# Performance work log

Hardware: AMD Instinct MI355X
Metric: run time of the kernel (lower is better)

## Reference

```python
import jax, jax.numpy as jnp
import numpy as np

MRG = 0.1
ALPHA = 32.0
STAT_WEIGHT = 0.01
STAT_ADJUST_WEIGHT = 0.15
COS_EPS = 1e-8  # torch F.cosine_similarity eps


def l2_norm(x):
    # matches torch l2_norm: x / sqrt(sum(x^2, axis=1) + 1e-12)
    normp = jnp.sum(x * x, axis=1) + 1e-12
    return x / jnp.sqrt(normp)[:, None]


def setup_inputs() -> dict:
    key = jax.random.key(0)
    kx, kt, kp, kc = jax.random.split(key, 4)
    B, C, D = 512, 50000, 128
    X = jax.random.normal(kx, (B, D), dtype=jnp.float32)
    T = jax.random.randint(kt, (B,), 0, C, dtype=jnp.int32)
    proxies = jax.random.normal(kp, (C, D), dtype=jnp.float32)
    class_centers = jax.random.normal(kc, (C, D), dtype=jnp.float32)
    return {"X": X, "T": T, "proxies": proxies, "class_centers": class_centers}


def reference(X, T, proxies, class_centers):
    C = proxies.shape[0]
    Xn = l2_norm(X)                      # (B, D)
    Pn = l2_norm(proxies)                # (C, D)
    cos = Xn @ Pn.T                      # (B, C)

    # ---- vectorized per-class statistics (replaces the Python loop) ----
    counts = jax.ops.segment_sum(jnp.ones(T.shape[0], jnp.float32), T, num_segments=C)
    sums = jax.ops.segment_sum(Xn, T, num_segments=C)          # (C, D)
    sqs = jax.ops.segment_sum(Xn * Xn, T, num_segments=C)      # (C, D)
    safe = jnp.maximum(counts, 1.0)[:, None]
    mean = sums / safe
    var = jnp.clip(sqs / safe - mean * mean, 1e-6, 10.0)        # biased var, clamped
    var_weight = 1.0 / (1.0 + var.mean(axis=1))                 # (C,)

    # cosine_similarity(P_norm[i], class_centers[i]) with torch eps semantics
    pnorm = jnp.maximum(jnp.sqrt(jnp.sum(Pn * Pn, axis=1)), COS_EPS)
    cnorm = jnp.maximum(jnp.sqrt(jnp.sum(class_centers * class_centers, axis=1)), COS_EPS)
    center_sim = jnp.sum(Pn * class_centers, axis=1) / (pnorm * cnorm)  # (C,)

    has_samples = counts > 0
    adj = jnp.where(has_samples, center_sim * var_weight * STAT_ADJUST_WEIGHT, 0.0)
    combined = cos + adj[None, :]        # (B, C)

    # ---- proxy-anchor exp-sum terms ----
    onehot = (T[:, None] == jnp.arange(C, dtype=T.dtype)[None, :])  # (B, C) bool
    pos_exp = jnp.exp(-ALPHA * (combined - MRG))
    neg_exp = jnp.exp(ALPHA * (combined + MRG))
    P_sim_sum = jnp.sum(jnp.where(onehot, pos_exp, 0.0), axis=0)    # (C,)
    N_sim_sum = jnp.sum(jnp.where(onehot, 0.0, neg_exp), axis=0)    # (C,)

    num_valid = jnp.sum(has_samples).astype(jnp.float32)
    pos_term = jnp.sum(jnp.log1p(P_sim_sum)) / num_valid
    neg_term = jnp.sum(jnp.log1p(N_sim_sum)) / jnp.float32(C)

    center_reg = jnp.mean(jnp.abs(class_centers))
    return pos_term + neg_term + STAT_WEIGHT * center_reg
```

## Files before the change

### kernel.cpp

```cpp
#include <hip/hip_runtime.h>
#include <math.h>

#define ALPHA 32.0f
#define MRG 0.1f
#define STAT_WEIGHT 0.01f
#define STAT_ADJ_W 0.15f
#define COS_EPS 1e-8f

typedef __attribute__((ext_vector_type(8))) short bf16x8;
typedef __attribute__((ext_vector_type(4))) float f32x4;
typedef __attribute__((ext_vector_type(4))) unsigned int u32x4;

__device__ __forceinline__ ushort f2bf(float f) {
    unsigned u = __float_as_uint(f);
    return (ushort)((u + 0x7FFFu + ((u >> 16) & 1u)) >> 16);
}
__device__ __forceinline__ unsigned pk2(float a, float b) {
    return (unsigned)f2bf(a) | ((unsigned)f2bf(b) << 16);
}

__device__ __forceinline__ float bred128(float v, float* sm, int d) {
    #pragma unroll
    for (int off = 1; off < 64; off <<= 1) v += __shfl_xor(v, off);
    if ((d & 63) == 0) sm[d >> 6] = v;
    __syncthreads();
    float r = sm[0] + sm[1];
    __syncthreads();
    return r;
}

__global__ void k_stats(const float* __restrict__ X, const float* __restrict__ proxies,
                        const float* __restrict__ cc, const int* __restrict__ T,
                        ushort* __restrict__ Xn16, float* __restrict__ adj,
                        float* __restrict__ scal, int B) {
    const int b = blockIdx.x, d = threadIdx.x;
    __shared__ int Tl[512];
    __shared__ float sm[2];
    __shared__ int mlist[512];
    __shared__ int mcnt;
    for (int i = d; i < B; i += 128) Tl[i] = T[i];
    if (d == 0) mcnt = 0;
    __syncthreads();
    const int c = Tl[b];

    float x = X[(size_t)b * 128 + d];
    float n2 = bred128(x * x, sm, d);
    float xn = x * rsqrtf(n2 + 1e-12f);
    const int pk = ((((d >> 3) ^ (b & 15)) << 3) | (d & 7));
    Xn16[(size_t)b * 128 + pk] = f2bf(xn);

    for (int j = d; j < B; j += 128)
        if (Tl[j] == c) mlist[atomicAdd(&mcnt, 1)] = j;
    __syncthreads();
    const int cnt = mcnt;
    int minj = mlist[0];
    for (int i = 1; i < cnt; ++i) minj = min(minj, mlist[i]);
    if (minj != b) return;

    float sd = 0.f, qd = 0.f;
    int prev = -1;
    for (int rank = 0; rank < cnt; ++rank) {
        int cur = 0x7fffffff;
        for (int i = 0; i < cnt; ++i) { int v = mlist[i]; if (v > prev && v < cur) cur = v; }
        prev = cur;
        float xj = X[(size_t)cur * 128 + d];
        float nj = bred128(xj * xj, sm, d);
        float xnj = xj * rsqrtf(nj + 1e-12f);
        sd += xnj; qd += xnj * xnj;
    }
    float fc = (float)cnt;
    float m = sd / fc;
    float var = fminf(fmaxf(qd / fc - m * m, 1e-6f), 10.0f);
    float sv = bred128(var, sm, d);

    float p  = proxies[(size_t)c * 128 + d];
    float cv = cc[(size_t)c * 128 + d];
    float s2 = bred128(p * p, sm, d);
    float c2 = bred128(cv * cv, sm, d);
    float pc = bred128(p * cv, sm, d);
    if (d == 0) {
        float inv = rsqrtf(s2 + 1e-12f);
        float pn = fmaxf(sqrtf(s2) * inv, COS_EPS);
        float cn = fmaxf(sqrtf(c2), COS_EPS);
        float censim = (pc * inv) / (pn * cn);
        float vw = 1.0f / (1.0f + sv * (1.0f / 128.0f));
        adj[c] = censim * vw * STAT_ADJ_W;
        atomicAdd(&scal[3], 1.0f);
    }
}

__launch_bounds__(256, 2)
__global__ void k_main(const float* __restrict__ proxies, const float* __restrict__ cc,
                       const ushort* __restrict__ Xsw, const int* __restrict__ T,
                       const float* __restrict__ adj, float* __restrict__ scal,
                       float* __restrict__ out, int C, int nblk) {
    const int tid = threadIdx.x, lane = tid & 63, wv = tid >> 6;
    const int nlo = lane & 15, quad = lane >> 4;
    const int c0 = blockIdx.x * 128;

    __shared__ ushort Sx[16384];
    __shared__ int Tl[512];
    __shared__ float red[4][3];
    Tl[tid] = T[tid];
    Tl[tid + 256] = T[tid + 256];

    float cabs = 0.f;
    {
        const int n4 = ((c0 + 128 <= C) ? 128 : (C - c0)) * 32;
        const float4* cp = (const float4*)(cc + (size_t)c0 * 128);
        #pragma unroll 4
        for (int i = tid; i < n4; i += 256) {
            float4 v = cp[i];
            cabs += fabsf(v.x) + fabsf(v.y) + fabsf(v.z) + fabsf(v.w);
        }
    }

    const int cls0 = c0 + wv * 32 + nlo;
    const int cls1 = cls0 + 16;
    bf16x8 bfr[2][4];
    #pragma unroll
    for (int t = 0; t < 2; ++t) {
        int cls = c0 + wv * 32 + t * 16 + nlo;
        int cl = (cls < C) ? cls : C - 1;
        const float4* pr = (const float4*)(proxies + (size_t)cl * 128);
        float4 v0[4], v1[4];
        float s2 = 0.f;
        #pragma unroll
        for (int ks = 0; ks < 4; ++ks) {
            v0[ks] = pr[ks * 8 + quad * 2];
            v1[ks] = pr[ks * 8 + quad * 2 + 1];
            s2 += v0[ks].x*v0[ks].x + v0[ks].y*v0[ks].y + v0[ks].z*v0[ks].z + v0[ks].w*v0[ks].w
                + v1[ks].x*v1[ks].x + v1[ks].y*v1[ks].y + v1[ks].z*v1[ks].z + v1[ks].w*v1[ks].w;
        }
        s2 += __shfl_xor(s2, 16);
        s2 += __shfl_xor(s2, 32);
        float pin = rsqrtf(s2 + 1e-12f);
        #pragma unroll
        for (int ks = 0; ks < 4; ++ks) {
            u32x4 u;
            u.x = pk2(v0[ks].x * pin, v0[ks].y * pin);
            u.y = pk2(v0[ks].z * pin, v0[ks].w * pin);
            u.z = pk2(v1[ks].x * pin, v1[ks].y * pin);
            u.w = pk2(v1[ks].z * pin, v1[ks].w * pin);
            bfr[t][ks] = __builtin_bit_cast(bf16x8, u);
        }
    }

    int fro[4];
    #pragma unroll
    for (int ks = 0; ks < 4; ++ks)
        fro[ks] = nlo * 128 + (((ks * 4 + quad) ^ nlo) << 3);

    const uint4* gX = (const uint4*)Xsw;
    uint4 s0, s1, s2v, s3;
    #define LOADV(ch) { const uint4* p_ = gX + (ch) * 1024 + tid; \
                        s0 = p_[0]; s1 = p_[256]; s2v = p_[512]; s3 = p_[768]; }
    #define WRITEV(bi) { uint4* q_ = (uint4*)&Sx[(bi) * 8192]; \
                         q_[tid] = s0; q_[tid + 256] = s1; q_[tid + 512] = s2v; q_[tid + 768] = s3; }
    LOADV(0); WRITEV(0); LOADV(1);
    __syncthreads();

    float pp0 = 0.f, np0 = 0.f, pp1 = 0.f, np1 = 0.f;
    for (int chunk = 0; chunk < 8; ++chunk) {
        const int bo = (chunk & 1) * 8192;
        if (chunk < 7) {
            WRITEV((chunk + 1) & 1);
            if (chunk < 6) LOADV(chunk + 2);
        }
        #pragma unroll
        for (int rt = 0; rt < 4; ++rt) {
            const ushort* sb = &Sx[bo + rt * 2048];
            bf16x8 a0 = *(const bf16x8*)&sb[fro[0]];
            bf16x8 a1 = *(const bf16x8*)&sb[fro[1]];
            bf16x8 a2 = *(const bf16x8*)&sb[fro[2]];
            bf16x8 a3 = *(const bf16x8*)&sb[fro[3]];
            f32x4 acc0 = {0.f,0.f,0.f,0.f}, acc1 = {0.f,0.f,0.f,0.f};
            acc0 = __builtin_amdgcn_mfma_f32_16x16x32_bf16(a0, bfr[0][0], acc0, 0, 0, 0);
            acc1 = __builtin_amdgcn_mfma_f32_16x16x32_bf16(a0, bfr[1][0], acc1, 0, 0, 0);
            acc0 = __builtin_amdgcn_mfma_f32_16x16x32_bf16(a1, bfr[0][1], acc0, 0, 0, 0);
            acc1 = __builtin_amdgcn_mfma_f32_16x16x32_bf16(a1, bfr[1][1], acc1, 0, 0, 0);
            acc0 = __builtin_amdgcn_mfma_f32_16x16x32_bf16(a2, bfr[0][2], acc0, 0, 0, 0);
            acc1 = __builtin_amdgcn_mfma_f32_16x16x32_bf16(a2, bfr[1][2], acc1, 0, 0, 0);
            acc0 = __builtin_amdgcn_mfma_f32_16x16x32_bf16(a3, bfr[0][3], acc0, 0, 0, 0);
            acc1 = __builtin_amdgcn_mfma_f32_16x16x32_bf16(a3, bfr[1][3], acc1, 0, 0, 0);

            int4 t4 = *(const int4*)&Tl[chunk * 64 + rt * 16 + quad * 4];
            int tvs[4] = {t4.x, t4.y, t4.z, t4.w};
            #pragma unroll
            for (int r = 0; r < 4; ++r) {
                { bool po = (tvs[r] == cls0); float v = acc0[r];
                  float e = __expf(po ? -ALPHA * (v - MRG) : ALPHA * (v + MRG));
                  pp0 += po ? e : 0.f; np0 += po ? 0.f : e; }
                { bool po = (tvs[r] == cls1); float v = acc1[r];
                  float e = __expf(po ? -ALPHA * (v - MRG) : ALPHA * (v + MRG));
                  pp1 += po ? e : 0.f; np1 += po ? 0.f : e; }
            }
        }
        __syncthreads();
    }
    #undef LOADV
    #undef WRITEV

    pp0 += __shfl_xor(pp0, 16); pp0 += __shfl_xor(pp0, 32);
    np0 += __shfl_xor(np0, 16); np0 += __shfl_xor(np0, 32);
    pp1 += __shfl_xor(pp1, 16); pp1 += __shfl_xor(pp1, 32);
    np1 += __shfl_xor(np1, 16); np1 += __shfl_xor(np1, 32);

    float lp = 0.f, ln = 0.f;
    {
        float a0 = adj[(cls0 < C) ? cls0 : C - 1];
        float a1 = adj[(cls1 < C) ? cls1 : C - 1];
        float as0 = (pp0 > 0.f) ? a0 : 0.f;
        float as1 = (pp1 > 0.f) ? a1 : 0.f;
        if (cls0 < C) {
            lp += log1pf(pp0 * __expf(-ALPHA * as0));
            ln += log1pf(np0 * __expf( ALPHA * as0));
        }
        if (cls1 < C) {
            lp += log1pf(pp1 * __expf(-ALPHA * as1));
            ln += log1pf(np1 * __expf( ALPHA * as1));
        }
    }
    #pragma unroll
    for (int off = 1; off < 16; off <<= 1) {
        lp += __shfl_xor(lp, off);
        ln += __shfl_xor(ln, off);
    }
    #pragma unroll
    for (int off = 1; off < 64; off <<= 1) cabs += __shfl_xor(cabs, off);

    if (lane == 0) { red[wv][0] = lp; red[wv][1] = ln; red[wv][2] = cabs; }
    __syncthreads();
    if (tid == 0) {
        atomicAdd(&scal[0], red[0][0] + red[1][0] + red[2][0] + red[3][0]);
        atomicAdd(&scal[1], red[0][1] + red[1][1] + red[2][1] + red[3][1]);
        atomicAdd(&scal[2], red[0][2] + red[1][2] + red[2][2] + red[3][2]);
        __threadfence();
        unsigned old = atomicAdd((unsigned*)(scal + 4), 1u);
        if (old == (unsigned)(nblk - 1)) {
            float S0 = atomicAdd(&scal[0], 0.f);
            float S1 = atomicAdd(&scal[1], 0.f);
            float S2 = atomicAdd(&scal[2], 0.f);
            float S3 = atomicAdd(&scal[3], 0.f);
            out[0] = S0 / S3 + S1 / (float)C + STAT_WEIGHT * (S2 / ((float)C * 128.f));
        }
    }
}

extern "C" void kernel_launch(void* const* d_in, const int* in_sizes, int n_in,
                              void* d_out, int out_size, void* d_ws, size_t ws_size,
                              hipStream_t stream) {
    const float* X       = (const float*)d_in[0];
    const int*   T       = (const int*)d_in[1];
    const float* proxies = (const float*)d_in[2];
    const float* cc      = (const float*)d_in[3];
    float* out = (float*)d_out;

    const int B = in_sizes[1];
    const int D = in_sizes[0] / B;
    const int C = in_sizes[2] / D;

    float*  adj  = (float*)d_ws;
    float*  scal = adj + C;
    ushort* Xn16 = (ushort*)(scal + 8);

    const int nblk = (C + 127) / 128;

    (void)hipMemsetAsync(scal, 0, 8 * sizeof(float), stream);
    k_stats<<<B, 128, 0, stream>>>(X, proxies, cc, T, Xn16, adj, scal, B);
    k_main<<<nblk, 256, 0, stream>>>(proxies, cc, Xn16, T, adj, scal, out, C, nblk);
}
```

Measured before the change: 133.5 us.

## Split batch rows across two grid halves with atomic partial sums and finalize kernel

The main kernel's grid gains a second dimension that splits the 512 batch rows into two halves of 256. Each block now processes 4 chunks instead of 8 and atomically adds its per-class positive and negative exp sums into global buffers. A new finalize kernel applies the log1p and adjustment terms per class and does the last reduction. This doubles block count, which should help occupancy across the CUs with 391 blocks originally. The cost is per-class atomics, a larger memset and an extra kernel launch, and the proxy normalization is now done twice.

```diff
diff --git a/kernel.cpp b/kernel.cpp
--- a/kernel.cpp
+++ b/kernel.cpp
@@ -92,20 +92,21 @@
 __launch_bounds__(256, 2)
 __global__ void k_main(const float* __restrict__ proxies, const float* __restrict__ cc,
                        const ushort* __restrict__ Xsw, const int* __restrict__ T,
-                       const float* __restrict__ adj, float* __restrict__ scal,
-                       float* __restrict__ out, int C, int nblk) {
+                       float* __restrict__ Psum, float* __restrict__ Nsum,
+                       float* __restrict__ scal, int C) {
     const int tid = threadIdx.x, lane = tid & 63, wv = tid >> 6;
     const int nlo = lane & 15, quad = lane >> 4;
     const int c0 = blockIdx.x * 128;
+    const int half = blockIdx.y;
+    const int r0 = half * 256;
 
     __shared__ ushort Sx[16384];
-    __shared__ int Tl[512];
-    __shared__ float red[4][3];
-    Tl[tid] = T[tid];
-    Tl[tid + 256] = T[tid + 256];
+    __shared__ alignas(16) int Tl[256];
+    __shared__ float red[4];
+    Tl[tid] = T[r0 + tid];
 
     float cabs = 0.f;
-    {
+    if (half == 0) {
         const int n4 = ((c0 + 128 <= C) ? 128 : (C - c0)) * 32;
         const float4* cp = (const float4*)(cc + (size_t)c0 * 128);
         #pragma unroll 4
@@ -151,7 +152,7 @@
     for (int ks = 0; ks < 4; ++ks)
         fro[ks] = nlo * 128 + (((ks * 4 + quad) ^ nlo) << 3);
 
-    const uint4* gX = (const uint4*)Xsw;
+    const uint4* gX = (const uint4*)Xsw + half * 4096;
     uint4 s0, s1, s2v, s3;
     #define LOADV(ch) { const uint4* p_ = gX + (ch) * 1024 + tid; \
                         s0 = p_[0]; s1 = p_[256]; s2v = p_[512]; s3 = p_[768]; }
@@ -161,11 +162,11 @@
     __syncthreads();
 
     float pp0 = 0.f, np0 = 0.f, pp1 = 0.f, np1 = 0.f;
-    for (int chunk = 0; chunk < 8; ++chunk) {
+    for (int chunk = 0; chunk < 4; ++chunk) {
         const int bo = (chunk & 1) * 8192;
-        if (chunk < 7) {
+        if (chunk < 3) {
             WRITEV((chunk + 1) & 1);
-            if (chunk < 6) LOADV(chunk + 2);
+            if (chunk < 2) LOADV(chunk + 2);
         }
         #pragma unroll
         for (int rt = 0; rt < 4; ++rt) {
@@ -205,39 +206,47 @@
     np0 += __shfl_xor(np0, 16); np0 += __shfl_xor(np0, 32);
     pp1 += __shfl_xor(pp1, 16); pp1 += __shfl_xor(pp1, 32);
     np1 += __shfl_xor(np1, 16); np1 += __shfl_xor(np1, 32);
-
+    if (quad == 0) {
+        if (cls0 < C) { atomicAdd(&Psum[cls0], pp0); atomicAdd(&Nsum[cls0], np0); }
+        if (cls1 < C) { atomicAdd(&Psum[cls1], pp1); atomicAdd(&Nsum[cls1], np1); }
+    }
+
+    if (half == 0) {
+        #pragma unroll
+        for (int off = 1; off < 64; off <<= 1) cabs += __shfl_xor(cabs, off);
+        if (lane == 0) red[wv] = cabs;
+        __syncthreads();
+        if (tid == 0) atomicAdd(&scal[2], red[0] + red[1] + red[2] + red[3]);
+    }
+}
+
+__launch_bounds__(256)
+__global__ void k_fin(const float* __restrict__ Psum, const float* __restrict__ Nsum,
+                      const float* __restrict__ adj, float* __restrict__ scal,
+                      float* __restrict__ out, int C, int nfin) {
+    const int tid = threadIdx.x, lane = tid & 63, wv = tid >> 6;
+    const int c = blockIdx.x * 256 + tid;
+    __shared__ float red[4][2];
     float lp = 0.f, ln = 0.f;
-    {
-        float a0 = adj[(cls0 < C) ? cls0 : C - 1];
-        float a1 = adj[(cls1 < C) ? cls1 : C - 1];
-        float as0 = (pp0 > 0.f) ? a0 : 0.f;
-        float as1 = (pp1 > 0.f) ? a1 : 0.f;
-        if (cls0 < C) {
-            lp += log1pf(pp0 * __expf(-ALPHA * as0));
-            ln += log1pf(np0 * __expf( ALPHA * as0));
-        }
-        if (cls1 < C) {
-            lp += log1pf(pp1 * __expf(-ALPHA * as1));
-            ln += log1pf(np1 * __expf( ALPHA * as1));
-        }
-    }
-    #pragma unroll
-    for (int off = 1; off < 16; off <<= 1) {
+    if (c < C) {
+        float p = Psum[c], n = Nsum[c];
+        float a = (p > 0.f) ? adj[c] : 0.f;
+        lp = log1pf(p * __expf(-ALPHA * a));
+        ln = log1pf(n * __expf( ALPHA * a));
+    }
+    #pragma unroll
+    for (int off = 1; off < 64; off <<= 1) {
         lp += __shfl_xor(lp, off);
         ln += __shfl_xor(ln, off);
     }
-    #pragma unroll
-    for (int off = 1; off < 64; off <<= 1) cabs += __shfl_xor(cabs, off);
-
-    if (lane == 0) { red[wv][0] = lp; red[wv][1] = ln; red[wv][2] = cabs; }
+    if (lane == 0) { red[wv][0] = lp; red[wv][1] = ln; }
     __syncthreads();
     if (tid == 0) {
         atomicAdd(&scal[0], red[0][0] + red[1][0] + red[2][0] + red[3][0]);
         atomicAdd(&scal[1], red[0][1] + red[1][1] + red[2][1] + red[3][1]);
-        atomicAdd(&scal[2], red[0][2] + red[1][2] + red[2][2] + red[3][2]);
         __threadfence();
         unsigned old = atomicAdd((unsigned*)(scal + 4), 1u);
-        if (old == (unsigned)(nblk - 1)) {
+        if (old == (unsigned)(nfin - 1)) {
             float S0 = atomicAdd(&scal[0], 0.f);
             float S1 = atomicAdd(&scal[1], 0.f);
             float S2 = atomicAdd(&scal[2], 0.f);
@@ -260,13 +269,17 @@
     const int D = in_sizes[0] / B;
     const int C = in_sizes[2] / D;
 
-    float*  adj  = (float*)d_ws;
-    float*  scal = adj + C;
-    ushort* Xn16 = (ushort*)(scal + 8);
+    float*  Psum = (float*)d_ws;
+    float*  Nsum = Psum + C;
+    float*  scal = Nsum + C;
+    float*  adj  = scal + 8;
+    ushort* Xn16 = (ushort*)(adj + C);
 
     const int nblk = (C + 127) / 128;
-
-    (void)hipMemsetAsync(scal, 0, 8 * sizeof(float), stream);
+    const int nfin = (C + 255) / 256;
+
+    (void)hipMemsetAsync(Psum, 0, (2 * (size_t)C + 8) * sizeof(float), stream);
     k_stats<<<B, 128, 0, stream>>>(X, proxies, cc, T, Xn16, adj, scal, B);
-    k_main<<<nblk, 256, 0, stream>>>(proxies, cc, Xn16, T, adj, scal, out, C, nblk);
-}
+    k_main<<<dim3(nblk, 2), 256, 0, stream>>>(proxies, cc, Xn16, T, Psum, Nsum, scal, C);
+    k_fin<<<nfin, 256, 0, stream>>>(Psum, Nsum, adj, scal, out, C, nfin);
+}
```

Result: no change. 135.7 us (+1.6%).
